# Performance work log

Measured on AMD Instinct MI355X. Metric: run time of the kernel, lower is better.

## Reference

```python
import jax, jax.numpy as jnp
import numpy as np

FANOUT = 8
N0_SRC, N0_DST = 1119744, 124416
N1_DST, N2_DST = 13824, 1536
D = 128


def setup_inputs() -> dict:
    key = jax.random.key(0)
    ks = jax.random.split(key, 20)
    s = 0.05
    inp = {
        'h': jax.random.normal(ks[0], (N0_SRC, D), jnp.float32),
        'es0': jax.random.randint(ks[1], (N0_DST * FANOUT,), 0, N0_SRC, jnp.int32),
        'es1': jax.random.randint(ks[2], (N1_DST * FANOUT,), 0, N0_DST, jnp.int32),
        'es2': jax.random.randint(ks[3], (N2_DST * FANOUT,), 0, N1_DST, jnp.int32),
        'Ws0': jax.random.normal(ks[4], (D, D), jnp.float32) * s,
        'Wn0': jax.random.normal(ks[5], (D, D), jnp.float32) * s,
        'bn0': jnp.zeros((D,), jnp.float32),
        'Ws1': jax.random.normal(ks[6], (D, D), jnp.float32) * s,
        'Wn1': jax.random.normal(ks[7], (D, D), jnp.float32) * s,
        'bn1': jnp.zeros((D,), jnp.float32),
        'Ws2': jax.random.normal(ks[8], (D, D), jnp.float32) * s,
        'Wn2': jax.random.normal(ks[9], (D, D), jnp.float32) * s,
        'bn2': jnp.zeros((D,), jnp.float32),
        'pW1': jax.random.normal(ks[10], (D, D), jnp.float32) * s,
        'pb1': jnp.zeros((D,), jnp.float32),
        'pW2': jax.random.normal(ks[11], (D, D), jnp.float32) * s,
        'pb2': jnp.zeros((D,), jnp.float32),
        'pW3': jax.random.normal(ks[12], (D, 1), jnp.float32) * s,
        'pb3': jnp.zeros((1,), jnp.float32),
    }
    return inp


def _sage_layer(h, es, n_dst, Ws, Wn, bn):
    # DGL SAGEConv 'mean': fc_self(h_dst) + fc_neigh(mean over sampled neighbors)
    # fixed fanout -> irregular gather then reshape-mean
    neigh = h[es].reshape(n_dst, FANOUT, h.shape[-1]).mean(axis=1)
    return h[:n_dst] @ Ws + neigh @ Wn + bn


def _predictor(x, pW1, pb1, pW2, pb2, pW3, pb3):
    x = jax.nn.relu(x @ pW1 + pb1)
    x = jax.nn.relu(x @ pW2 + pb2)
    return x @ pW3 + pb3


def reference(h, es0, es1, es2, Ws0, Wn0, bn0, Ws1, Wn1, bn1, Ws2, Wn2, bn2,
              pW1, pb1, pW2, pb2, pW3, pb3):
    h1 = jax.nn.relu(_sage_layer(h, es0, N0_DST, Ws0, Wn0, bn0))
    h2 = jax.nn.relu(_sage_layer(h1, es1, N1_DST, Ws1, Wn1, bn1))
    h3 = _sage_layer(h2, es2, N2_DST, Ws2, Wn2, bn2)  # no relu on last layer
    src_h, pos_h, neg_h = jnp.split(h3, 3, axis=0)
    h_pos = _predictor(src_h * pos_h, pW1, pb1, pW2, pb2, pW3, pb3)
    h_neg = _predictor(src_h * neg_h, pW1, pb1, pW2, pb2, pW3, pb3)
    return h_pos, h_neg
```

## Files before the change

### kernel.cpp

```cpp
#include <hip/hip_runtime.h>
#include <cstddef>

#define DD 128
#define FAN 8

__device__ __forceinline__ void lds_fence() {
    asm volatile("s_waitcnt lgkmcnt(0)" ::: "memory");
}

template<bool RELU, int R>
__global__ __launch_bounds__(512, 2)
void sage_kernel(const float* __restrict__ X, const int* __restrict__ es,
                 const float* __restrict__ Ws, const float* __restrict__ Wn,
                 const float* __restrict__ bn, float* __restrict__ Y,
                 int n_dst, int n_groups)
{
    __shared__ float sW[2 * DD][DD];
    __shared__ float sx[8][R][2 * DD];

    const int tid  = threadIdx.x;
    const int lane = tid & 63;
    const int wave = tid >> 6;

    {
        const float4* s0 = (const float4*)Ws;
        const float4* s1 = (const float4*)Wn;
        float4* dst = (float4*)&sW[0][0];
        #pragma unroll
        for (int i = 0; i < 8; ++i) dst[tid + 512 * i] = s0[tid + 512 * i];
        #pragma unroll
        for (int i = 0; i < 8; ++i) dst[4096 + tid + 512 * i] = s1[tid + 512 * i];
    }
    __syncthreads();

    const float2 bv = *((const float2*)bn + lane);

    for (int g = blockIdx.x; g < n_groups; g += gridDim.x) {
        const int row0 = g * (8 * R) + wave * R;

        #pragma unroll
        for (int rr = 0; rr < R; ++rr) {
            const int r = row0 + rr;
            if (r >= n_dst) continue;
            const int* ep = es + (size_t)r * FAN;
            float a0 = 0.f, a1 = 0.f;
            #pragma unroll
            for (int j = 0; j < FAN; ++j) {
                const int sj = ep[j];
                const float2 v = *((const float2*)(X + (size_t)sj * DD) + lane);
                a0 += v.x; a1 += v.y;
            }
            const float2 sv = *((const float2*)(X + (size_t)r * DD) + lane);
            *(float2*)&sx[wave][rr][2 * lane] = sv;
            *(float2*)&sx[wave][rr][DD + 2 * lane] = make_float2(a0 * 0.125f, a1 * 0.125f);
        }
        lds_fence();

        float2 acc[R];
        #pragma unroll
        for (int rr = 0; rr < R; ++rr) acc[rr] = make_float2(0.f, 0.f);

        #pragma unroll 8
        for (int k = 0; k < 2 * DD; k += 2) {
            const float2 w0 = *((const float2*)&sW[k][0]     + lane);
            const float2 w1 = *((const float2*)&sW[k + 1][0] + lane);
            #pragma unroll
            for (int rr = 0; rr < R; ++rr) {
                const float2 xv = *(const float2*)&sx[wave][rr][k];
                acc[rr].x = fmaf(xv.x, w0.x, acc[rr].x);
                acc[rr].y = fmaf(xv.x, w0.y, acc[rr].y);
                acc[rr].x = fmaf(xv.y, w1.x, acc[rr].x);
                acc[rr].y = fmaf(xv.y, w1.y, acc[rr].y);
            }
        }

        #pragma unroll
        for (int rr = 0; rr < R; ++rr) {
            const int r = row0 + rr;
            if (r >= n_dst) continue;
            float o0 = acc[rr].x + bv.x;
            float o1 = acc[rr].y + bv.y;
            if (RELU) { o0 = fmaxf(o0, 0.f); o1 = fmaxf(o1, 0.f); }
            *((float2*)(Y + (size_t)r * DD) + lane) = make_float2(o0, o1);
        }
        lds_fence();
    }
}

__global__ __launch_bounds__(512, 2)
void pred_kernel(const float* __restrict__ h3,
                 const float* __restrict__ W1, const float* __restrict__ b1,
                 const float* __restrict__ W2, const float* __restrict__ b2,
                 const float* __restrict__ W3, const float* __restrict__ b3,
                 float* __restrict__ out)
{
    __shared__ float sW1[DD][DD];
    __shared__ float sW2[DD][DD];
    __shared__ float sW3[DD];
    __shared__ float sx[8][4][DD];

    const int tid = threadIdx.x, lane = tid & 63, wave = tid >> 6;
    {
        const float4* a = (const float4*)W1;  float4* d1 = (float4*)&sW1[0][0];
        const float4* c = (const float4*)W2;  float4* d2 = (float4*)&sW2[0][0];
        #pragma unroll
        for (int i = 0; i < 8; ++i) d1[tid + 512 * i] = a[tid + 512 * i];
        #pragma unroll
        for (int i = 0; i < 8; ++i) d2[tid + 512 * i] = c[tid + 512 * i];
        if (tid < DD) sW3[tid] = W3[tid];
    }
    __syncthreads();

    const int row0 = blockIdx.x * 32 + wave * 4;

    #pragma unroll
    for (int rr = 0; rr < 4; ++rr) {
        const int row = row0 + rr;
        const int i = row & 511;
        const int which = row >> 9;
        const float2 a = *((const float2*)(h3 + (size_t)i * DD) + lane);
        const float2 c = *((const float2*)(h3 + (size_t)(512 + which * 512 + i) * DD) + lane);
        *(float2*)&sx[wave][rr][2 * lane] = make_float2(a.x * c.x, a.y * c.y);
    }
    lds_fence();

    float2 t[4];
    #pragma unroll
    for (int rr = 0; rr < 4; ++rr) t[rr] = make_float2(0.f, 0.f);
    #pragma unroll 8
    for (int k = 0; k < DD; k += 2) {
        const float2 w0 = *((const float2*)&sW1[k][0]     + lane);
        const float2 w1 = *((const float2*)&sW1[k + 1][0] + lane);
        #pragma unroll
        for (int rr = 0; rr < 4; ++rr) {
            const float2 xv = *(const float2*)&sx[wave][rr][k];
            t[rr].x = fmaf(xv.x, w0.x, t[rr].x);
            t[rr].y = fmaf(xv.x, w0.y, t[rr].y);
            t[rr].x = fmaf(xv.y, w1.x, t[rr].x);
            t[rr].y = fmaf(xv.y, w1.y, t[rr].y);
        }
    }
    const float2 b1v = *((const float2*)b1 + lane);
    lds_fence();
    #pragma unroll
    for (int rr = 0; rr < 4; ++rr) {
        const float u0 = fmaxf(t[rr].x + b1v.x, 0.f);
        const float u1 = fmaxf(t[rr].y + b1v.y, 0.f);
        *(float2*)&sx[wave][rr][2 * lane] = make_float2(u0, u1);
    }
    lds_fence();

    #pragma unroll
    for (int rr = 0; rr < 4; ++rr) t[rr] = make_float2(0.f, 0.f);
    #pragma unroll 8
    for (int k = 0; k < DD; k += 2) {
        const float2 w0 = *((const float2*)&sW2[k][0]     + lane);
        const float2 w1 = *((const float2*)&sW2[k + 1][0] + lane);
        #pragma unroll
        for (int rr = 0; rr < 4; ++rr) {
            const float2 xv = *(const float2*)&sx[wave][rr][k];
            t[rr].x = fmaf(xv.x, w0.x, t[rr].x);
            t[rr].y = fmaf(xv.x, w0.y, t[rr].y);
            t[rr].x = fmaf(xv.y, w1.x, t[rr].x);
            t[rr].y = fmaf(xv.y, w1.y, t[rr].y);
        }
    }
    const float2 b2v = *((const float2*)b2 + lane);
    const float bias3 = b3[0];

    #pragma unroll
    for (int rr = 0; rr < 4; ++rr) {
        const float u0 = fmaxf(t[rr].x + b2v.x, 0.f);
        const float u1 = fmaxf(t[rr].y + b2v.y, 0.f);
        float p = u0 * sW3[2 * lane] + u1 * sW3[2 * lane + 1];
        #pragma unroll
        for (int off = 32; off > 0; off >>= 1) p += __shfl_down(p, off);
        if (lane == 0) out[row0 + rr] = p + bias3;
    }
}

extern "C" void kernel_launch(void* const* d_in, const int* in_sizes, int n_in,
                              void* d_out, int out_size, void* d_ws, size_t ws_size,
                              hipStream_t stream)
{
    const float* h   = (const float*)d_in[0];
    const int*   es0 = (const int*)d_in[1];
    const int*   es1 = (const int*)d_in[2];
    const int*   es2 = (const int*)d_in[3];
    const float* Ws0 = (const float*)d_in[4];
    const float* Wn0 = (const float*)d_in[5];
    const float* bn0 = (const float*)d_in[6];
    const float* Ws1 = (const float*)d_in[7];
    const float* Wn1 = (const float*)d_in[8];
    const float* bn1 = (const float*)d_in[9];
    const float* Ws2 = (const float*)d_in[10];
    const float* Wn2 = (const float*)d_in[11];
    const float* bn2 = (const float*)d_in[12];
    const float* pW1 = (const float*)d_in[13];
    const float* pb1 = (const float*)d_in[14];
    const float* pW2 = (const float*)d_in[15];
    const float* pb2 = (const float*)d_in[16];
    const float* pW3 = (const float*)d_in[17];
    const float* pb3 = (const float*)d_in[18];
    float* out = (float*)d_out;

    char* ws = (char*)d_ws;
    float* h1 = (float*)(ws);
    float* h2 = (float*)(ws + 63700992);
    float* h3 = (float*)(ws + 63700992 + 7077888);

    sage_kernel<true, 3><<<512, 512, 0, stream>>>(h,  es0, Ws0, Wn0, bn0, h1, 124416, 5184);
    sage_kernel<true, 3><<<512, 512, 0, stream>>>(h1, es1, Ws1, Wn1, bn1, h2, 13824, 576);
    sage_kernel<false,3><<<64,  512, 0, stream>>>(h2, es2, Ws2, Wn2, bn2, h3, 1536, 64);
    pred_kernel<<<32, 512, 0, stream>>>(h3, pW1, pb1, pW2, pb2, pW3, pb3, out);
}
```

Before: 906.7 us.

## Broadcast activations via readlane and interleave weights for float4 LDS reads

The SAGE kernel no longer stages per-row self and neighbor-mean vectors in LDS. Each lane keeps its two feature values in registers, and the GEMV broadcasts them with v_readlane. Weights are repacked in LDS so that one float4 load serves two k rows. Rows per wave are raised (8/4/2 per layer), bounds checks are dropped, and grids are resized so the groups divide exactly. This removes LDS traffic for activations and raises weight reuse, at the cost of more scalar readlane work and register pressure, and it relies on the row counts dividing exactly.

```diff
diff --git a/kernel.cpp b/kernel.cpp
--- a/kernel.cpp
+++ b/kernel.cpp
@@ -6,6 +6,10 @@
 
 __device__ __forceinline__ void lds_fence() {
     asm volatile("s_waitcnt lgkmcnt(0)" ::: "memory");
+}
+
+__device__ __forceinline__ float rlane(float v, int l) {
+    return __int_as_float(__builtin_amdgcn_readlane(__float_as_int(v), l));
 }
 
 template<bool RELU, int R>
@@ -13,77 +17,86 @@
 void sage_kernel(const float* __restrict__ X, const int* __restrict__ es,
                  const float* __restrict__ Ws, const float* __restrict__ Wn,
                  const float* __restrict__ bn, float* __restrict__ Y,
-                 int n_dst, int n_groups)
+                 int n_groups)
 {
-    __shared__ float sW[2 * DD][DD];
-    __shared__ float sx[8][R][2 * DD];
+    __shared__ float sW[2 * DD * DD];
 
     const int tid  = threadIdx.x;
     const int lane = tid & 63;
     const int wave = tid >> 6;
 
-    {
-        const float4* s0 = (const float4*)Ws;
-        const float4* s1 = (const float4*)Wn;
-        float4* dst = (float4*)&sW[0][0];
-        #pragma unroll
-        for (int i = 0; i < 8; ++i) dst[tid + 512 * i] = s0[tid + 512 * i];
-        #pragma unroll
-        for (int i = 0; i < 8; ++i) dst[4096 + tid + 512 * i] = s1[tid + 512 * i];
+    #pragma unroll
+    for (int i = 0; i < 32; ++i) {
+        const int idx = i * 512 + tid;
+        const int k = idx >> 6, l = idx & 63;
+        const float2 v = (k < DD)
+            ? *((const float2*)(Ws + (size_t)k * DD) + l)
+            : *((const float2*)(Wn + (size_t)(k - DD) * DD) + l);
+        *(float2*)&sW[(k >> 1) * 256 + l * 4 + (k & 1) * 2] = v;
     }
     __syncthreads();
 
     const float2 bv = *((const float2*)bn + lane);
+    const float4* sWv = (const float4*)sW;
 
     for (int g = blockIdx.x; g < n_groups; g += gridDim.x) {
-        const int row0 = g * (8 * R) + wave * R;
-
+        const int row0 = (g * 8 + wave) * R;
+
+        float s0[R], s1[R], m0[R], m1[R];
         #pragma unroll
         for (int rr = 0; rr < R; ++rr) {
             const int r = row0 + rr;
-            if (r >= n_dst) continue;
             const int* ep = es + (size_t)r * FAN;
-            float a0 = 0.f, a1 = 0.f;
+            const float2 sv = *((const float2*)(X + (size_t)r * DD) + lane);
+            float g0 = 0.f, g1 = 0.f;
             #pragma unroll
             for (int j = 0; j < FAN; ++j) {
-                const int sj = ep[j];
-                const float2 v = *((const float2*)(X + (size_t)sj * DD) + lane);
-                a0 += v.x; a1 += v.y;
+                const float2 v = *((const float2*)(X + (size_t)ep[j] * DD) + lane);
+                g0 += v.x; g1 += v.y;
             }
-            const float2 sv = *((const float2*)(X + (size_t)r * DD) + lane);
-            *(float2*)&sx[wave][rr][2 * lane] = sv;
-            *(float2*)&sx[wave][rr][DD + 2 * lane] = make_float2(a0 * 0.125f, a1 * 0.125f);
-        }
-        lds_fence();
-
-        float2 acc[R];
-        #pragma unroll
-        for (int rr = 0; rr < R; ++rr) acc[rr] = make_float2(0.f, 0.f);
-
-        #pragma unroll 8
-        for (int k = 0; k < 2 * DD; k += 2) {
-            const float2 w0 = *((const float2*)&sW[k][0]     + lane);
-            const float2 w1 = *((const float2*)&sW[k + 1][0] + lane);
+            s0[rr] = sv.x; s1[rr] = sv.y;
+            m0[rr] = g0 * 0.125f; m1[rr] = g1 * 0.125f;
+        }
+
+        float acc0[R], acc1[R];
+        #pragma unroll
+        for (int rr = 0; rr < R; ++rr) { acc0[rr] = 0.f; acc1[rr] = 0.f; }
+
+        #pragma unroll 2
+        for (int kp = 0; kp < 64; ++kp) {
+            const float4 w = sWv[kp * 64 + lane];
             #pragma unroll
             for (int rr = 0; rr < R; ++rr) {
-                const float2 xv = *(const float2*)&sx[wave][rr][k];
-                acc[rr].x = fmaf(xv.x, w0.x, acc[rr].x);
-                acc[rr].y = fmaf(xv.x, w0.y, acc[rr].y);
-                acc[rr].x = fmaf(xv.y, w1.x, acc[rr].x);
-                acc[rr].y = fmaf(xv.y, w1.y, acc[rr].y);
+                const float xa = rlane(s0[rr], kp);
+                const float xb = rlane(s1[rr], kp);
+                acc0[rr] = fmaf(xa, w.x, acc0[rr]);
+                acc1[rr] = fmaf(xa, w.y, acc1[rr]);
+                acc0[rr] = fmaf(xb, w.z, acc0[rr]);
+                acc1[rr] = fmaf(xb, w.w, acc1[rr]);
+            }
+        }
+        #pragma unroll 2
+        for (int kp = 64; kp < 128; ++kp) {
+            const float4 w = sWv[kp * 64 + lane];
+            #pragma unroll
+            for (int rr = 0; rr < R; ++rr) {
+                const float xa = rlane(m0[rr], kp - 64);
+                const float xb = rlane(m1[rr], kp - 64);
+                acc0[rr] = fmaf(xa, w.x, acc0[rr]);
+                acc1[rr] = fmaf(xa, w.y, acc1[rr]);
+                acc0[rr] = fmaf(xb, w.z, acc0[rr]);
+                acc1[rr] = fmaf(xb, w.w, acc1[rr]);
             }
         }
 
         #pragma unroll
         for (int rr = 0; rr < R; ++rr) {
             const int r = row0 + rr;
-            if (r >= n_dst) continue;
-            float o0 = acc[rr].x + bv.x;
-            float o1 = acc[rr].y + bv.y;
+            float o0 = acc0[rr] + bv.x;
+            float o1 = acc1[rr] + bv.y;
             if (RELU) { o0 = fmaxf(o0, 0.f); o1 = fmaxf(o1, 0.f); }
             *((float2*)(Y + (size_t)r * DD) + lane) = make_float2(o0, o1);
         }
-        lds_fence();
     }
 }
 
@@ -209,8 +222,8 @@
     float* h2 = (float*)(ws + 63700992);
     float* h3 = (float*)(ws + 63700992 + 7077888);
 
-    sage_kernel<true, 3><<<512, 512, 0, stream>>>(h,  es0, Ws0, Wn0, bn0, h1, 124416, 5184);
-    sage_kernel<true, 3><<<512, 512, 0, stream>>>(h1, es1, Ws1, Wn1, bn1, h2, 13824, 576);
-    sage_kernel<false,3><<<64,  512, 0, stream>>>(h2, es2, Ws2, Wn2, bn2, h3, 1536, 64);
+    sage_kernel<true, 8><<<512, 512, 0, stream>>>(h,  es0, Ws0, Wn0, bn0, h1, 1944);
+    sage_kernel<true, 4><<<432, 512, 0, stream>>>(h1, es1, Ws1, Wn1, bn1, h2, 432);
+    sage_kernel<false,2><<<96,  512, 0, stream>>>(h2, es2, Ws2, Wn2, bn2, h3, 96);
     pred_kernel<<<32, 512, 0, stream>>>(h3, pW1, pb1, pW2, pb2, pW3, pb3, out);
 }
```

New measurement: 929.6 us. +2.5%, slower.
